# Kernel optimization log

Measured on AMD Instinct MI355X. Metric: run time of the kernel, lower is better.

The kernel has to match this reference:

```python
import jax, jax.numpy as jnp
import numpy as np

N_NODES = 100000
N_EDGES = 1280000
D_IN = 64
D_HID = 64
D_OUT = 1
N_GRAPHS = 512


def setup_inputs() -> dict:
    key = jax.random.key(0)
    ks = jax.random.split(key, 12)
    x = jax.random.normal(ks[0], (N_NODES, D_IN), dtype=jnp.float32)
    edge_index = jax.random.randint(ks[1], (2, N_EDGES), 0, N_NODES, dtype=jnp.int32)
    batch = jnp.sort(jax.random.randint(ks[2], (N_NODES,), 0, N_GRAPHS, dtype=jnp.int32))
    s = 0.1
    w0 = jax.random.normal(ks[3], (D_IN, D_HID), dtype=jnp.float32) * s
    b0 = jnp.zeros((D_HID,), dtype=jnp.float32)
    w1 = jax.random.normal(ks[4], (D_HID, D_HID), dtype=jnp.float32) * s
    b1 = jnp.zeros((D_HID,), dtype=jnp.float32)
    w2 = jax.random.normal(ks[5], (D_HID, D_HID), dtype=jnp.float32) * s
    b2 = jnp.zeros((D_HID,), dtype=jnp.float32)
    fc_w = jax.random.normal(ks[6], (D_HID, D_OUT), dtype=jnp.float32) * s
    fc_b = jnp.zeros((D_OUT,), dtype=jnp.float32)
    return {"x": x, "edge_index": edge_index, "batch": batch,
            "w0": w0, "b0": b0, "w1": w1, "b1": b1, "w2": w2, "b2": b2,
            "fc_w": fc_w, "fc_b": fc_b}


def _gcn_conv(x, w, b, src, dst):
    # PyG GCNConv: h = x @ W; out_i = sum_j norm_ij * h_j over (A + I), sym norm.
    h = x @ w                                           # [N, H]
    ones = jnp.ones((src.shape[0],), dtype=h.dtype)
    deg = jax.ops.segment_sum(ones, dst, num_segments=N_NODES) + 1.0  # +1 self-loop
    dinv = jax.lax.rsqrt(deg)                           # [N]
    norm = dinv[src] * dinv[dst]                        # [E]
    agg = jax.ops.segment_sum(h[src] * norm[:, None], dst, num_segments=N_NODES)
    agg = agg + h * (dinv * dinv)[:, None]              # self-loop term
    return agg + b


def reference(x, edge_index, batch, w0, b0, w1, b1, w2, b2, fc_w, fc_b):
    src, dst = edge_index[0], edge_index[1]
    # 3 stacked GCNConv + relu (dropout is identity in eval mode)
    h = jax.nn.relu(_gcn_conv(x, w0, b0, src, dst))
    h = jax.nn.relu(_gcn_conv(h, w1, b1, src, dst))
    h = jax.nn.relu(_gcn_conv(h, w2, b2, src, dst))
    # global mean pool per graph
    sums = jax.ops.segment_sum(h, batch, num_segments=N_GRAPHS)        # [G, H]
    cnt = jax.ops.segment_sum(jnp.ones((N_NODES,), h.dtype), batch, num_segments=N_GRAPHS)
    mean = sums / jnp.maximum(cnt, 1.0)[:, None]
    return mean @ fc_w + fc_b                            # [G, 1]
```

## Files before the change

### kernel.cpp

```cpp
#include <hip/hip_runtime.h>
#include <hip/hip_fp16.h>
#include <type_traits>

#define N_NODES 100000
#define N_EDGES 1280000
#define N_GRAPHS 512
#define NBK 196
#define CHUNK 3200
#define NCH 400
#define CAP 8192

typedef _Float16 v8h __attribute__((ext_vector_type(8)));
typedef float v4f __attribute__((ext_vector_type(4)));

__device__ inline void fmix_lo(float& acc, unsigned h2, float n) {
    asm volatile("v_fma_mix_f32 %0, %1, %2, %0 op_sel:[0,0,0] op_sel_hi:[1,0,0]"
                 : "+v"(acc) : "v"(h2), "v"(n));
}
__device__ inline void fmix_hi(float& acc, unsigned h2, float n) {
    asm volatile("v_fma_mix_f32 %0, %1, %2, %0 op_sel:[1,0,0] op_sel_hi:[1,0,0]"
                 : "+v"(acc) : "v"(h2), "v"(n));
}


__global__ __launch_bounds__(256) void edge_scatter(const int* __restrict__ src,
                                                    const int* __restrict__ dst,
                                                    int* __restrict__ bcur,
                                                    int2* __restrict__ pairs) {
    __shared__ int2 buf[CHUNK];
    __shared__ int lcnt[NBK], lloc[NBK], lcur[NBK];
    __shared__ int s[256];
    int t = threadIdx.x;
    for (int k = t; k < NBK; k += 256) { lcnt[k] = 0; lcur[k] = 0; }
    __syncthreads();
    int e0 = blockIdx.x * CHUNK;
    for (int i = t; i < CHUNK; i += 256) atomicAdd(&lcnt[dst[e0 + i] >> 9], 1);
    __syncthreads();
    {
        int v = (t < NBK) ? lcnt[t] : 0;
        s[t] = v; __syncthreads();
        for (int d = 1; d < 256; d <<= 1) {
            int x = (t >= d) ? s[t - d] : 0;
            __syncthreads();
            s[t] += x;
            __syncthreads();
        }
        if (t < NBK) lloc[t] = s[t] - v;
    }
    __syncthreads();
    for (int i = t; i < CHUNK; i += 256) {
        int d = dst[e0 + i];
        int k = d >> 9;
        int li = lloc[k] + atomicAdd(&lcur[k], 1);
        buf[li] = make_int2(src[e0 + i], d);
    }
    __syncthreads();
    for (int k = t; k < NBK; k += 256) {
        int c = lcnt[k];
        if (c) {
            int g = atomicAdd(&bcur[k * 16], c);
            int lo = lloc[k];
            int2* dstp = pairs + (size_t)k * CAP;
            for (int j = 0; j < c; j++)
                if (g + j < CAP) dstp[g + j] = buf[lo + j];
        }
    }
}


__global__ void bucket_scan(const int* __restrict__ bcur, int* __restrict__ bbase,
                            int* __restrict__ offs) {
    __shared__ int s[256];
    int t = threadIdx.x;
    int v = (t < NBK) ? min(bcur[t * 16], CAP) : 0;
    s[t] = v; __syncthreads();
    for (int d = 1; d < 256; d <<= 1) {
        int x = (t >= d) ? s[t - d] : 0;
        __syncthreads();
        s[t] += x;
        __syncthreads();
    }
    if (t < NBK) bbase[t] = s[t] - v;
    if (t == 0) offs[N_NODES] = N_EDGES;
}


__global__ __launch_bounds__(512) void bucket_place(const int2* __restrict__ pairs,
                                                    const int* __restrict__ bbase,
                                                    const int* __restrict__ bcur,
                                                    int* __restrict__ offs,
                                                    float* __restrict__ dinv,
                                                    int* __restrict__ csr) {
    __shared__ int lcnt[512];
    __shared__ int lofs[512];
    __shared__ int lcur[512];
    __shared__ int lsrc[CAP];
    int t = threadIdx.x;
    int b = blockIdx.x;
    int node0 = b << 9;
    int nn = min(512, N_NODES - node0);
    int beg = bbase[b];
    int cnt = min(bcur[b * 16], CAP);
    const int2* prs = pairs + (size_t)b * CAP;
    lcnt[t] = 0; lcur[t] = 0;
    __syncthreads();
    for (int i = t; i < cnt; i += 512)
        atomicAdd(&lcnt[prs[i].y - node0], 1);
    __syncthreads();
    int deg = lcnt[t];
    for (int d = 1; d < 512; d <<= 1) {
        int x = (t >= d) ? lcnt[t - d] : 0;
        __syncthreads();
        lcnt[t] += x;
        __syncthreads();
    }
    lofs[t] = lcnt[t] - deg;
    if (t < nn) {
        offs[node0 + t] = beg + lcnt[t] - deg;
        dinv[node0 + t] = 1.0f / sqrtf((float)deg + 1.0f);
    }
    __syncthreads();
    for (int i = t; i < cnt; i += 512) {
        int2 pr = prs[i];
        int n = pr.y - node0;
        int li = lofs[n] + atomicAdd(&lcur[n], 1);
        if (li < CAP) lsrc[li] = pr.x << 4;
    }
    __syncthreads();
    for (int j = t; j < cnt; j += 512) csr[beg + j] = lsrc[j];
}


template <typename T>
__global__ __launch_bounds__(256) void gemm_mfma(const T* __restrict__ X,
                                                 const float* __restrict__ W,
                                                 const float* __restrict__ dinv,
                                                 __half* __restrict__ H) {
    __shared__ _Float16 Wt[64][72];
    int t = threadIdx.x;
    {
        #pragma unroll
        for (int q = 0; q < 4; q++) {
            int idx = t + q * 256;
            int k = idx >> 4;
            int n0 = (idx & 15) * 4;
            float4 v = ((const float4*)W)[idx];
            Wt[n0 + 0][k] = (_Float16)v.x;
            Wt[n0 + 1][k] = (_Float16)v.y;
            Wt[n0 + 2][k] = (_Float16)v.z;
            Wt[n0 + 3][k] = (_Float16)v.w;
        }
    }
    __syncthreads();

    int wv = t >> 6, lane = t & 63;
    int m = lane & 15, quad = lane >> 4;

    v8h bf[4][2];
    #pragma unroll
    for (int c = 0; c < 4; c++)
        #pragma unroll
        for (int h = 0; h < 2; h++)
            bf[c][h] = *(const v8h*)&Wt[c * 16 + m][h * 32 + quad * 8];

    int base = blockIdx.x * 256 + wv * 64;
    #pragma unroll
    for (int tt = 0; tt < 4; tt++) {
        int tile = base + tt * 16;
        int rA = min(tile + m, N_NODES - 1);
        v8h a0, a1;
        if constexpr (std::is_same<T, float>::value) {
            const float* xp = (const float*)X + (size_t)rA * 64 + quad * 8;
            float4 p0 = *(const float4*)xp;
            float4 p1 = *(const float4*)(xp + 4);
            float4 p2 = *(const float4*)(xp + 32);
            float4 p3 = *(const float4*)(xp + 36);
            a0 = (v8h){(_Float16)p0.x, (_Float16)p0.y, (_Float16)p0.z, (_Float16)p0.w,
                       (_Float16)p1.x, (_Float16)p1.y, (_Float16)p1.z, (_Float16)p1.w};
            a1 = (v8h){(_Float16)p2.x, (_Float16)p2.y, (_Float16)p2.z, (_Float16)p2.w,
                       (_Float16)p3.x, (_Float16)p3.y, (_Float16)p3.z, (_Float16)p3.w};
        } else {
            const _Float16* xp = (const _Float16*)X + (size_t)rA * 64 + quad * 8;
            a0 = *(const v8h*)xp;
            a1 = *(const v8h*)(xp + 32);
        }
        v4f acc[4];
        #pragma unroll
        for (int c = 0; c < 4; c++) {
            acc[c] = (v4f){0.f, 0.f, 0.f, 0.f};
            acc[c] = __builtin_amdgcn_mfma_f32_16x16x32_f16(a0, bf[c][0], acc[c], 0, 0, 0);
            acc[c] = __builtin_amdgcn_mfma_f32_16x16x32_f16(a1, bf[c][1], acc[c], 0, 0, 0);
        }
        #pragma unroll
        for (int r = 0; r < 4; r++) {
            int row = tile + quad * 4 + r;
            if (row < N_NODES) {
                float dv = dinv[row];
                __half* hp = H + (size_t)row * 64 + m;
                #pragma unroll
                for (int c = 0; c < 4; c++)
                    hp[c * 16] = __float2half(acc[c][r] * dv);
            }
        }
    }
}


__device__ inline void agg_body(const uint2* __restrict__ Hh, int wid, int lane,
                                const int* __restrict__ offs,
                                const int* __restrict__ csr,
                                const float* __restrict__ dinv,
                                float4& out) {
    int eg = lane >> 4;
    int fq = lane & 15;
    int beg = offs[wid], end = offs[wid + 1];
    float di = dinv[wid];
    uint2 us = Hh[wid * 16 + fq];

    float4 a0 = {0.f, 0.f, 0.f, 0.f};
    float4 a1 = {0.f, 0.f, 0.f, 0.f};
    for (int base = beg; base < end; base += 16) {
        int i0 = base + eg;
        int r0 = csr[i0], r1 = csr[i0 + 4], r2 = csr[i0 + 8], r3 = csr[i0 + 12];
        bool p0 = i0      < end, p1 = i0 + 4  < end,
             p2 = i0 + 8  < end, p3 = i0 + 12 < end;
        int s0 = p0 ? r0 : 0, s1 = p1 ? r1 : 0,
            s2 = p2 ? r2 : 0, s3 = p3 ? r3 : 0;
        uint2 u0 = Hh[s0 + fq];
        uint2 u1 = Hh[s1 + fq];
        uint2 u2 = Hh[s2 + fq];
        uint2 u3 = Hh[s3 + fq];
        float n0 = p0 ? di : 0.f;
        float n1 = p1 ? di : 0.f;
        float n2 = p2 ? di : 0.f;
        float n3 = p3 ? di : 0.f;
        fmix_lo(a0.x, u0.x, n0); fmix_hi(a0.y, u0.x, n0);
        fmix_lo(a0.z, u0.y, n0); fmix_hi(a0.w, u0.y, n0);
        fmix_lo(a1.x, u1.x, n1); fmix_hi(a1.y, u1.x, n1);
        fmix_lo(a1.z, u1.y, n1); fmix_hi(a1.w, u1.y, n1);
        fmix_lo(a0.x, u2.x, n2); fmix_hi(a0.y, u2.x, n2);
        fmix_lo(a0.z, u2.y, n2); fmix_hi(a0.w, u2.y, n2);
        fmix_lo(a1.x, u3.x, n3); fmix_hi(a1.y, u3.x, n3);
        fmix_lo(a1.z, u3.y, n3); fmix_hi(a1.w, u3.y, n3);
    }
    a0.x += a1.x; a0.y += a1.y; a0.z += a1.z; a0.w += a1.w;
    a0.x += __shfl_xor(a0.x, 16); a0.y += __shfl_xor(a0.y, 16);
    a0.z += __shfl_xor(a0.z, 16); a0.w += __shfl_xor(a0.w, 16);
    a0.x += __shfl_xor(a0.x, 32); a0.y += __shfl_xor(a0.y, 32);
    a0.z += __shfl_xor(a0.z, 32); a0.w += __shfl_xor(a0.w, 32);
    float2 s01 = __half22float2(*(__half2*)&us.x);
    float2 s23 = __half22float2(*(__half2*)&us.y);
    out.x = a0.x + s01.x * di; out.y = a0.y + s01.y * di;
    out.z = a0.z + s23.x * di; out.w = a0.w + s23.y * di;
}

__global__ __launch_bounds__(256) void agg_gcn(const __half* __restrict__ H,
                                               const int* __restrict__ offs,
                                               const int* __restrict__ csr,
                                               const float* __restrict__ dinv,
                                               const float* __restrict__ bias,
                                               __half* __restrict__ Out) {
    int wid = (blockIdx.x * 256 + threadIdx.x) >> 6;
    int lane = threadIdx.x & 63;
    if (wid >= N_NODES) return;
    float4 r;
    agg_body((const uint2*)H, wid, lane, offs, csr, dinv, r);
    int fq = lane & 15;
    if ((lane >> 4) == 0) {
        float4 b4 = ((const float4*)bias)[fq];
        __half2 h01 = __float22half2_rn(make_float2(fmaxf(r.x + b4.x, 0.f),
                                                    fmaxf(r.y + b4.y, 0.f)));
        __half2 h23 = __float22half2_rn(make_float2(fmaxf(r.z + b4.z, 0.f),
                                                    fmaxf(r.w + b4.w, 0.f)));
        uint2 u;
        u.x = *(unsigned int*)&h01;
        u.y = *(unsigned int*)&h23;
        ((uint2*)Out)[(size_t)wid * 16 + fq] = u;
    }
}

__global__ __launch_bounds__(256) void agg_gcn_pool(const __half* __restrict__ H,
                                                    const int* __restrict__ offs,
                                                    const int* __restrict__ csr,
                                                    const float* __restrict__ dinv,
                                                    const float* __restrict__ bias,
                                                    const float* __restrict__ fcw,
                                                    float* __restrict__ p) {
    int wid = (blockIdx.x * 256 + threadIdx.x) >> 6;
    int lane = threadIdx.x & 63;
    if (wid >= N_NODES) return;
    float4 r;
    agg_body((const uint2*)H, wid, lane, offs, csr, dinv, r);
    int fq = lane & 15;
    float4 b4 = ((const float4*)bias)[fq];
    float4 f4 = ((const float4*)fcw)[fq];
    float v = fmaxf(r.x + b4.x, 0.f) * f4.x + fmaxf(r.y + b4.y, 0.f) * f4.y
            + fmaxf(r.z + b4.z, 0.f) * f4.z + fmaxf(r.w + b4.w, 0.f) * f4.w;
    v += __shfl_xor(v, 1); v += __shfl_xor(v, 2);
    v += __shfl_xor(v, 4); v += __shfl_xor(v, 8);
    if (lane == 0) p[wid] = v;
}


__device__ inline int lower_bound_batch(const int* __restrict__ batch, int key) {
    int lo = 0, hi = N_NODES;
    while (lo < hi) {
        int mid = (lo + hi) >> 1;
        if (batch[mid] < key) lo = mid + 1; else hi = mid;
    }
    return lo;
}

__global__ __launch_bounds__(256) void graph_reduce(const float* __restrict__ p,
                                                    const int* __restrict__ batch,
                                                    const float* __restrict__ fcb,
                                                    float* __restrict__ out) {
    __shared__ float red[4];
    int g = blockIdx.x;
    int s0 = lower_bound_batch(batch, g);
    int s1 = lower_bound_batch(batch, g + 1);
    float acc = 0.f;
    for (int i = s0 + threadIdx.x; i < s1; i += 256) acc += p[i];
    #pragma unroll
    for (int o = 32; o > 0; o >>= 1) acc += __shfl_xor(acc, o);
    int lane = threadIdx.x & 63, wv = threadIdx.x >> 6;
    if (lane == 0) red[wv] = acc;
    __syncthreads();
    if (threadIdx.x == 0) {
        float sum = red[0] + red[1] + red[2] + red[3];
        out[g] = sum / fmaxf((float)(s1 - s0), 1.f) + fcb[0];
    }
}


extern "C" void kernel_launch(void* const* d_in, const int* in_sizes, int n_in,
                              void* d_out, int out_size, void* d_ws, size_t ws_size,
                              hipStream_t stream) {
    const float* x    = (const float*)d_in[0];
    const int*   ei   = (const int*)d_in[1];
    const int*   batch= (const int*)d_in[2];
    const float* w0   = (const float*)d_in[3];
    const float* b0   = (const float*)d_in[4];
    const float* w1   = (const float*)d_in[5];
    const float* b1   = (const float*)d_in[6];
    const float* w2   = (const float*)d_in[7];
    const float* b2   = (const float*)d_in[8];
    const float* fcw  = (const float*)d_in[9];
    const float* fcb  = (const float*)d_in[10];
    float* out = (float*)d_out;

    const int* src_e = ei;
    const int* dst_e = ei + N_EDGES;

    char* w = (char*)d_ws;
    size_t o = 0;
    int*    bcur  = (int*)(w + o);    o += 256 * 16 * 4;
    int*    bbase = (int*)(w + o);    o += 256 * 4;
    int*    offs  = (int*)(w + o);    o += (size_t)(N_NODES + 8) * 4;
    float*  dinv  = (float*)(w + o);  o += (size_t)N_NODES * 4;
    int2*   pairs = (int2*)(w + o);   o += (size_t)NBK * CAP * 8;
    int*    csr   = (int*)(w + o);    o += (size_t)(N_EDGES + 16) * 4;
    __half* bufA  = (__half*)(w + o); o += (size_t)N_NODES * 64 * 2;
    __half* bufB  = (__half*)(w + o); o += (size_t)N_NODES * 64 * 2;
    float*  pvec  = (float*)(w + o);  o += (size_t)N_NODES * 4;

    hipMemsetAsync(bcur, 0, 256 * 16 * 4, stream);
    hipMemsetAsync(csr + N_EDGES, 0, 16 * 4, stream);

    edge_scatter<<<NCH, 256, 0, stream>>>(src_e, dst_e, bcur, pairs);
    bucket_scan<<<1, 256, 0, stream>>>(bcur, bbase, offs);
    bucket_place<<<NBK, 512, 0, stream>>>(pairs, bbase, bcur, offs, dinv, csr);

    const int GEMM_BLOCKS = (N_NODES + 255) / 256;
    const int AGG_BLOCKS  = (N_NODES + 3) / 4;

    gemm_mfma<float><<<GEMM_BLOCKS, 256, 0, stream>>>(x, w0, dinv, bufA);
    agg_gcn<<<AGG_BLOCKS, 256, 0, stream>>>(bufA, offs, csr, dinv, b0, bufB);

    gemm_mfma<__half><<<GEMM_BLOCKS, 256, 0, stream>>>(bufB, w1, dinv, bufA);
    agg_gcn<<<AGG_BLOCKS, 256, 0, stream>>>(bufA, offs, csr, dinv, b1, bufB);

    gemm_mfma<__half><<<GEMM_BLOCKS, 256, 0, stream>>>(bufB, w2, dinv, bufA);
    agg_gcn_pool<<<AGG_BLOCKS, 256, 0, stream>>>(bufA, offs, csr, dinv, b2, fcw, pvec);

    graph_reduce<<<N_GRAPHS, 256, 0, stream>>>(pvec, batch, fcb, out);
}
```

Measured before the change: 295.9 us.

## Fuse edge scatter with first GEMM and fold bucket scan into split placement

The first-layer GEMM no longer depends on dinv. Its blocks are appended to the edge-scatter launch so both run concurrently in one kernel. Because those GEMM outputs are not prescaled, the first aggregation multiplies in the dinv of each source node itself. The separate bucket_scan kernel is removed: each placement block computes its bucket base with an in-block reduction, and each bucket is split across two 256-thread blocks. The trade-offs are an extra dinv gather per edge in layer one, redundant base reductions in every placement block, and a smaller per-half CSR capacity (CAPH) that risks overflow on skewed degree distributions.

New measurement: 292.3 us. No clear change (-1.2%).

```diff
diff --git a/kernel.cpp b/kernel.cpp
--- a/kernel.cpp
+++ b/kernel.cpp
@@ -9,6 +9,8 @@
 #define CHUNK 3200
 #define NCH 400
 #define CAP 8192
+#define CAPH 4096
+#define GEMM_BLOCKS 391
 
 typedef _Float16 v8h __attribute__((ext_vector_type(8)));
 typedef float v4f __attribute__((ext_vector_type(4)));
@@ -23,133 +25,23 @@
 }
 
 
-__global__ __launch_bounds__(256) void edge_scatter(const int* __restrict__ src,
-                                                    const int* __restrict__ dst,
-                                                    int* __restrict__ bcur,
-                                                    int2* __restrict__ pairs) {
-    __shared__ int2 buf[CHUNK];
-    __shared__ int lcnt[NBK], lloc[NBK], lcur[NBK];
-    __shared__ int s[256];
+template <typename T, bool FOLD>
+__device__ inline void gemm_body(int bid, const T* __restrict__ X,
+                                 const float* __restrict__ W,
+                                 const float* __restrict__ dinv,
+                                 __half* __restrict__ H,
+                                 _Float16 (*Wt)[72]) {
     int t = threadIdx.x;
-    for (int k = t; k < NBK; k += 256) { lcnt[k] = 0; lcur[k] = 0; }
-    __syncthreads();
-    int e0 = blockIdx.x * CHUNK;
-    for (int i = t; i < CHUNK; i += 256) atomicAdd(&lcnt[dst[e0 + i] >> 9], 1);
-    __syncthreads();
-    {
-        int v = (t < NBK) ? lcnt[t] : 0;
-        s[t] = v; __syncthreads();
-        for (int d = 1; d < 256; d <<= 1) {
-            int x = (t >= d) ? s[t - d] : 0;
-            __syncthreads();
-            s[t] += x;
-            __syncthreads();
-        }
-        if (t < NBK) lloc[t] = s[t] - v;
-    }
-    __syncthreads();
-    for (int i = t; i < CHUNK; i += 256) {
-        int d = dst[e0 + i];
-        int k = d >> 9;
-        int li = lloc[k] + atomicAdd(&lcur[k], 1);
-        buf[li] = make_int2(src[e0 + i], d);
-    }
-    __syncthreads();
-    for (int k = t; k < NBK; k += 256) {
-        int c = lcnt[k];
-        if (c) {
-            int g = atomicAdd(&bcur[k * 16], c);
-            int lo = lloc[k];
-            int2* dstp = pairs + (size_t)k * CAP;
-            for (int j = 0; j < c; j++)
-                if (g + j < CAP) dstp[g + j] = buf[lo + j];
-        }
-    }
-}
-
-
-__global__ void bucket_scan(const int* __restrict__ bcur, int* __restrict__ bbase,
-                            int* __restrict__ offs) {
-    __shared__ int s[256];
-    int t = threadIdx.x;
-    int v = (t < NBK) ? min(bcur[t * 16], CAP) : 0;
-    s[t] = v; __syncthreads();
-    for (int d = 1; d < 256; d <<= 1) {
-        int x = (t >= d) ? s[t - d] : 0;
-        __syncthreads();
-        s[t] += x;
-        __syncthreads();
-    }
-    if (t < NBK) bbase[t] = s[t] - v;
-    if (t == 0) offs[N_NODES] = N_EDGES;
-}
-
-
-__global__ __launch_bounds__(512) void bucket_place(const int2* __restrict__ pairs,
-                                                    const int* __restrict__ bbase,
-                                                    const int* __restrict__ bcur,
-                                                    int* __restrict__ offs,
-                                                    float* __restrict__ dinv,
-                                                    int* __restrict__ csr) {
-    __shared__ int lcnt[512];
-    __shared__ int lofs[512];
-    __shared__ int lcur[512];
-    __shared__ int lsrc[CAP];
-    int t = threadIdx.x;
-    int b = blockIdx.x;
-    int node0 = b << 9;
-    int nn = min(512, N_NODES - node0);
-    int beg = bbase[b];
-    int cnt = min(bcur[b * 16], CAP);
-    const int2* prs = pairs + (size_t)b * CAP;
-    lcnt[t] = 0; lcur[t] = 0;
-    __syncthreads();
-    for (int i = t; i < cnt; i += 512)
-        atomicAdd(&lcnt[prs[i].y - node0], 1);
-    __syncthreads();
-    int deg = lcnt[t];
-    for (int d = 1; d < 512; d <<= 1) {
-        int x = (t >= d) ? lcnt[t - d] : 0;
-        __syncthreads();
-        lcnt[t] += x;
-        __syncthreads();
-    }
-    lofs[t] = lcnt[t] - deg;
-    if (t < nn) {
-        offs[node0 + t] = beg + lcnt[t] - deg;
-        dinv[node0 + t] = 1.0f / sqrtf((float)deg + 1.0f);
-    }
-    __syncthreads();
-    for (int i = t; i < cnt; i += 512) {
-        int2 pr = prs[i];
-        int n = pr.y - node0;
-        int li = lofs[n] + atomicAdd(&lcur[n], 1);
-        if (li < CAP) lsrc[li] = pr.x << 4;
-    }
-    __syncthreads();
-    for (int j = t; j < cnt; j += 512) csr[beg + j] = lsrc[j];
-}
-
-
-template <typename T>
-__global__ __launch_bounds__(256) void gemm_mfma(const T* __restrict__ X,
-                                                 const float* __restrict__ W,
-                                                 const float* __restrict__ dinv,
-                                                 __half* __restrict__ H) {
-    __shared__ _Float16 Wt[64][72];
-    int t = threadIdx.x;
-    {
-        #pragma unroll
-        for (int q = 0; q < 4; q++) {
-            int idx = t + q * 256;
-            int k = idx >> 4;
-            int n0 = (idx & 15) * 4;
-            float4 v = ((const float4*)W)[idx];
-            Wt[n0 + 0][k] = (_Float16)v.x;
-            Wt[n0 + 1][k] = (_Float16)v.y;
-            Wt[n0 + 2][k] = (_Float16)v.z;
-            Wt[n0 + 3][k] = (_Float16)v.w;
-        }
+    #pragma unroll
+    for (int q = 0; q < 4; q++) {
+        int idx = t + q * 256;
+        int k = idx >> 4;
+        int n0 = (idx & 15) * 4;
+        float4 v = ((const float4*)W)[idx];
+        Wt[n0 + 0][k] = (_Float16)v.x;
+        Wt[n0 + 1][k] = (_Float16)v.y;
+        Wt[n0 + 2][k] = (_Float16)v.z;
+        Wt[n0 + 3][k] = (_Float16)v.w;
     }
     __syncthreads();
 
@@ -163,7 +55,7 @@
         for (int h = 0; h < 2; h++)
             bf[c][h] = *(const v8h*)&Wt[c * 16 + m][h * 32 + quad * 8];
 
-    int base = blockIdx.x * 256 + wv * 64;
+    int base = bid * 256 + wv * 64;
     #pragma unroll
     for (int tt = 0; tt < 4; tt++) {
         int tile = base + tt * 16;
@@ -195,17 +87,149 @@
         for (int r = 0; r < 4; r++) {
             int row = tile + quad * 4 + r;
             if (row < N_NODES) {
-                float dv = dinv[row];
+                float dv = FOLD ? dinv[row] : 1.0f;
                 __half* hp = H + (size_t)row * 64 + m;
                 #pragma unroll
                 for (int c = 0; c < 4; c++)
-                    hp[c * 16] = __float2half(acc[c][r] * dv);
+                    hp[c * 16] = __float2half(FOLD ? acc[c][r] * dv : acc[c][r]);
             }
         }
     }
 }
 
-
+template <typename T, bool FOLD>
+__global__ __launch_bounds__(256) void gemm_mfma(const T* __restrict__ X,
+                                                 const float* __restrict__ W,
+                                                 const float* __restrict__ dinv,
+                                                 __half* __restrict__ H) {
+    __shared__ _Float16 Wt[64][72];
+    gemm_body<T, FOLD>(blockIdx.x, X, W, dinv, H, Wt);
+}
+
+
+#define SC_BUF   0
+#define SC_LCNT  (CHUNK * 8)
+#define SC_LLOC  (SC_LCNT + NBK * 4)
+#define SC_LCUR  (SC_LLOC + NBK * 4)
+#define SC_S     (SC_LCUR + NBK * 4)
+#define SC_BYTES (SC_S + 256 * 4)
+
+__global__ __launch_bounds__(256) void scatter_gemm(const int* __restrict__ src,
+                                                    const int* __restrict__ dst,
+                                                    int* __restrict__ bcur,
+                                                    int2* __restrict__ pairs,
+                                                    const float* __restrict__ x,
+                                                    const float* __restrict__ w0,
+                                                    __half* __restrict__ H) {
+    alignas(16) __shared__ char smem[SC_BYTES];
+    if (blockIdx.x >= NCH) {
+        gemm_body<float, false>(blockIdx.x - NCH, x, w0, nullptr, H,
+                                (_Float16(*)[72])smem);
+        return;
+    }
+    int2* buf  = (int2*)(smem + SC_BUF);
+    int*  lcnt = (int*)(smem + SC_LCNT);
+    int*  lloc = (int*)(smem + SC_LLOC);
+    int*  lcur = (int*)(smem + SC_LCUR);
+    int*  s    = (int*)(smem + SC_S);
+    int t = threadIdx.x;
+    for (int k = t; k < NBK; k += 256) { lcnt[k] = 0; lcur[k] = 0; }
+    __syncthreads();
+    int e0 = blockIdx.x * CHUNK;
+    for (int i = t; i < CHUNK; i += 256) atomicAdd(&lcnt[dst[e0 + i] >> 9], 1);
+    __syncthreads();
+    {
+        int v = (t < NBK) ? lcnt[t] : 0;
+        s[t] = v; __syncthreads();
+        for (int d = 1; d < 256; d <<= 1) {
+            int xx = (t >= d) ? s[t - d] : 0;
+            __syncthreads();
+            s[t] += xx;
+            __syncthreads();
+        }
+        if (t < NBK) lloc[t] = s[t] - v;
+    }
+    __syncthreads();
+    for (int i = t; i < CHUNK; i += 256) {
+        int d = dst[e0 + i];
+        int k = d >> 9;
+        int li = lloc[k] + atomicAdd(&lcur[k], 1);
+        buf[li] = make_int2(src[e0 + i], d);
+    }
+    __syncthreads();
+    for (int k = t; k < NBK; k += 256) {
+        int c = lcnt[k];
+        if (c) {
+            int g = atomicAdd(&bcur[k * 16], c);
+            int lo = lloc[k];
+            int2* dstp = pairs + (size_t)k * CAP;
+            for (int j = 0; j < c; j++)
+                if (g + j < CAP) dstp[g + j] = buf[lo + j];
+        }
+    }
+}
+
+
+__global__ __launch_bounds__(256) void bucket_place(const int2* __restrict__ pairs,
+                                                    const int* __restrict__ bcur,
+                                                    int* __restrict__ offs,
+                                                    float* __restrict__ dinv,
+                                                    int* __restrict__ csr) {
+    __shared__ int lcnt[256], lofs[256], lcur[256], red[256];
+    __shared__ int lsrc[CAPH];
+    int t = threadIdx.x;
+    int bb = blockIdx.x;
+    int b = bb >> 1, half = bb & 1;
+    int node0 = (b << 9) + (half << 8);
+    int nn = min(256, N_NODES - node0);
+    red[t] = (t < b) ? min(bcur[t * 16], CAP) : 0;
+    __syncthreads();
+    for (int d = 128; d > 0; d >>= 1) {
+        if (t < d) red[t] += red[t + d];
+        __syncthreads();
+    }
+    int bbase = red[0];
+    int cnt = min(bcur[b * 16], CAP);
+    __syncthreads();
+    lcnt[t] = 0; lcur[t] = 0;
+    __syncthreads();
+    const int2* prs = pairs + (size_t)b * CAP;
+    for (int i = t; i < cnt; i += 256) {
+        int n = prs[i].y - (b << 9);
+        if ((n >> 8) == half) atomicAdd(&lcnt[n & 255], 1);
+    }
+    __syncthreads();
+    int deg = lcnt[t];
+    red[t] = deg; __syncthreads();
+    for (int d = 1; d < 256; d <<= 1) {
+        int xx = (t >= d) ? red[t - d] : 0;
+        __syncthreads();
+        red[t] += xx;
+        __syncthreads();
+    }
+    lofs[t] = red[t] - deg;
+    int total = red[255];
+    int beg = bbase + (half ? (cnt - total) : 0);
+    if (t < nn) {
+        offs[node0 + t] = beg + lofs[t];
+        dinv[node0 + t] = 1.0f / sqrtf((float)deg + 1.0f);
+    }
+    __syncthreads();
+    for (int i = t; i < cnt; i += 256) {
+        int2 pr = prs[i];
+        int n = pr.y - (b << 9);
+        if ((n >> 8) == half) {
+            int li = lofs[n & 255] + atomicAdd(&lcur[n & 255], 1);
+            if (li < CAPH) lsrc[li] = pr.x;
+        }
+    }
+    __syncthreads();
+    for (int j = t; j < total; j += 256) csr[beg + j] = lsrc[j];
+    if (bb == 0 && t == 0) offs[N_NODES] = N_EDGES;
+}
+
+
+template <bool FULL>
 __device__ inline void agg_body(const uint2* __restrict__ Hh, int wid, int lane,
                                 const int* __restrict__ offs,
                                 const int* __restrict__ csr,
@@ -226,14 +250,23 @@
              p2 = i0 + 8  < end, p3 = i0 + 12 < end;
         int s0 = p0 ? r0 : 0, s1 = p1 ? r1 : 0,
             s2 = p2 ? r2 : 0, s3 = p3 ? r3 : 0;
-        uint2 u0 = Hh[s0 + fq];
-        uint2 u1 = Hh[s1 + fq];
-        uint2 u2 = Hh[s2 + fq];
-        uint2 u3 = Hh[s3 + fq];
-        float n0 = p0 ? di : 0.f;
-        float n1 = p1 ? di : 0.f;
-        float n2 = p2 ? di : 0.f;
-        float n3 = p3 ? di : 0.f;
+        uint2 u0 = Hh[(s0 << 4) + fq];
+        uint2 u1 = Hh[(s1 << 4) + fq];
+        uint2 u2 = Hh[(s2 << 4) + fq];
+        uint2 u3 = Hh[(s3 << 4) + fq];
+        float n0, n1, n2, n3;
+        if constexpr (FULL) {
+            float d0 = dinv[s0], d1 = dinv[s1], d2 = dinv[s2], d3 = dinv[s3];
+            n0 = p0 ? d0 * di : 0.f;
+            n1 = p1 ? d1 * di : 0.f;
+            n2 = p2 ? d2 * di : 0.f;
+            n3 = p3 ? d3 * di : 0.f;
+        } else {
+            n0 = p0 ? di : 0.f;
+            n1 = p1 ? di : 0.f;
+            n2 = p2 ? di : 0.f;
+            n3 = p3 ? di : 0.f;
+        }
         fmix_lo(a0.x, u0.x, n0); fmix_hi(a0.y, u0.x, n0);
         fmix_lo(a0.z, u0.y, n0); fmix_hi(a0.w, u0.y, n0);
         fmix_lo(a1.x, u1.x, n1); fmix_hi(a1.y, u1.x, n1);
@@ -250,10 +283,12 @@
     a0.z += __shfl_xor(a0.z, 32); a0.w += __shfl_xor(a0.w, 32);
     float2 s01 = __half22float2(*(__half2*)&us.x);
     float2 s23 = __half22float2(*(__half2*)&us.y);
-    out.x = a0.x + s01.x * di; out.y = a0.y + s01.y * di;
-    out.z = a0.z + s23.x * di; out.w = a0.w + s23.y * di;
-}
-
+    float sw = FULL ? di * di : di;
+    out.x = a0.x + s01.x * sw; out.y = a0.y + s01.y * sw;
+    out.z = a0.z + s23.x * sw; out.w = a0.w + s23.y * sw;
+}
+
+template <bool FULL>
 __global__ __launch_bounds__(256) void agg_gcn(const __half* __restrict__ H,
                                                const int* __restrict__ offs,
                                                const int* __restrict__ csr,
@@ -264,7 +299,7 @@
     int lane = threadIdx.x & 63;
     if (wid >= N_NODES) return;
     float4 r;
-    agg_body((const uint2*)H, wid, lane, offs, csr, dinv, r);
+    agg_body<FULL>((const uint2*)H, wid, lane, offs, csr, dinv, r);
     int fq = lane & 15;
     if ((lane >> 4) == 0) {
         float4 b4 = ((const float4*)bias)[fq];
@@ -290,7 +325,7 @@
     int lane = threadIdx.x & 63;
     if (wid >= N_NODES) return;
     float4 r;
-    agg_body((const uint2*)H, wid, lane, offs, csr, dinv, r);
+    agg_body<false>((const uint2*)H, wid, lane, offs, csr, dinv, r);
     int fq = lane & 15;
     float4 b4 = ((const float4*)bias)[fq];
     float4 f4 = ((const float4*)fcw)[fq];
@@ -355,7 +390,6 @@
     char* w = (char*)d_ws;
     size_t o = 0;
     int*    bcur  = (int*)(w + o);    o += 256 * 16 * 4;
-    int*    bbase = (int*)(w + o);    o += 256 * 4;
     int*    offs  = (int*)(w + o);    o += (size_t)(N_NODES + 8) * 4;
     float*  dinv  = (float*)(w + o);  o += (size_t)N_NODES * 4;
     int2*   pairs = (int2*)(w + o);   o += (size_t)NBK * CAP * 8;
@@ -365,22 +399,19 @@
     float*  pvec  = (float*)(w + o);  o += (size_t)N_NODES * 4;
 
     hipMemsetAsync(bcur, 0, 256 * 16 * 4, stream);
-    hipMemsetAsync(csr + N_EDGES, 0, 16 * 4, stream);
-
-    edge_scatter<<<NCH, 256, 0, stream>>>(src_e, dst_e, bcur, pairs);
-    bucket_scan<<<1, 256, 0, stream>>>(bcur, bbase, offs);
-    bucket_place<<<NBK, 512, 0, stream>>>(pairs, bbase, bcur, offs, dinv, csr);
-
-    const int GEMM_BLOCKS = (N_NODES + 255) / 256;
-    const int AGG_BLOCKS  = (N_NODES + 3) / 4;
-
-    gemm_mfma<float><<<GEMM_BLOCKS, 256, 0, stream>>>(x, w0, dinv, bufA);
-    agg_gcn<<<AGG_BLOCKS, 256, 0, stream>>>(bufA, offs, csr, dinv, b0, bufB);
-
-    gemm_mfma<__half><<<GEMM_BLOCKS, 256, 0, stream>>>(bufB, w1, dinv, bufA);
-    agg_gcn<<<AGG_BLOCKS, 256, 0, stream>>>(bufA, offs, csr, dinv, b1, bufB);
-
-    gemm_mfma<__half><<<GEMM_BLOCKS, 256, 0, stream>>>(bufB, w2, dinv, bufA);
+
+    const int AGG_BLOCKS = (N_NODES + 3) / 4;
+
+    scatter_gemm<<<NCH + GEMM_BLOCKS, 256, 0, stream>>>(src_e, dst_e, bcur, pairs,
+                                                        x, w0, bufA);
+    bucket_place<<<2 * NBK, 256, 0, stream>>>(pairs, bcur, offs, dinv, csr);
+
+    agg_gcn<true><<<AGG_BLOCKS, 256, 0, stream>>>(bufA, offs, csr, dinv, b0, bufB);
+
+    gemm_mfma<__half, true><<<GEMM_BLOCKS, 256, 0, stream>>>(bufB, w1, dinv, bufA);
+    agg_gcn<false><<<AGG_BLOCKS, 256, 0, stream>>>(bufA, offs, csr, dinv, b1, bufB);
+
+    gemm_mfma<__half, true><<<GEMM_BLOCKS, 256, 0, stream>>>(bufB, w2, dinv, bufA);
     agg_gcn_pool<<<AGG_BLOCKS, 256, 0, stream>>>(bufA, offs, csr, dinv, b2, fcw, pvec);
 
     graph_reduce<<<N_GRAPHS, 256, 0, stream>>>(pvec, batch, fcb, out);
```
